# Kernel optimization log

Measured on AMD Instinct MI355X. Metric: run time of the kernel, lower is better.

Reference implementation:

```python
import jax, jax.numpy as jnp
import numpy as np

B, T = 256, 64
STOCH, DETER, HIDDEN = 32, 1024, 1024
EMBED, ACT, ENS = 1536, 6, 5
MIN_STD = 0.1
UPDATE_BIAS = -1.0
LN_EPS = 1e-5


def _layernorm(x, g, b):
    m = jnp.mean(x, -1, keepdims=True)
    v = jnp.var(x, -1, keepdims=True)
    return (x - m) * jax.lax.rsqrt(v + LN_EPS) * g + b


def setup_inputs() -> dict:
    key = jax.random.key(0)
    ks = jax.random.split(key, 24)
    s = 0.02
    return {
        "embed": jax.random.normal(ks[0], (B, T, EMBED), jnp.float32),
        "action": jax.random.normal(ks[1], (B, T, ACT), jnp.float32),
        "eps_post": jax.random.normal(ks[2], (B, T, STOCH), jnp.float32),
        "eps_prior": jax.random.normal(ks[3], (B, T, STOCH), jnp.float32),
        "is_first": jnp.zeros((B, T), bool),
        "ens_idx": jax.random.randint(ks[4], (T,), 0, ENS, jnp.int32),
        # GRU cell: Linear(hidden+deter -> 3*deter) + LayerNorm(3*deter)
        "W_gru": s * jax.random.normal(ks[5], (HIDDEN + DETER, 3 * DETER), jnp.float32),
        "b_gru": jnp.zeros((3 * DETER,), jnp.float32),
        "ln_g": jnp.ones((3 * DETER,), jnp.float32),
        "ln_b": jnp.zeros((3 * DETER,), jnp.float32),
        # img_inp: Linear(stoch+act -> hidden)
        "W_inp": s * jax.random.normal(ks[6], (STOCH + ACT, HIDDEN), jnp.float32),
        "b_inp": jnp.zeros((HIDDEN,), jnp.float32),
        # obs_out: Linear(deter+embed -> hidden)
        "W_obs": s * jax.random.normal(ks[7], (DETER + EMBED, HIDDEN), jnp.float32),
        "b_obs": jnp.zeros((HIDDEN,), jnp.float32),
        # ensemble img_out heads: Linear(deter -> hidden) x ENS
        "W_ens": s * jax.random.normal(ks[8], (ENS, DETER, HIDDEN), jnp.float32),
        "b_ens": jnp.zeros((ENS, HIDDEN), jnp.float32),
        # dist layers: Linear(hidden -> 2*stoch)
        "W_obs_dist": s * jax.random.normal(ks[9], (HIDDEN, 2 * STOCH), jnp.float32),
        "b_obs_dist": jnp.zeros((2 * STOCH,), jnp.float32),
        "W_ens_dist": s * jax.random.normal(ks[10], (ENS, HIDDEN, 2 * STOCH), jnp.float32),
        "b_ens_dist": jnp.zeros((ENS, 2 * STOCH), jnp.float32),
    }


def _observe(embed, action, eps_post, eps_prior, is_first, ens_idx,
             W_gru, b_gru, ln_g, ln_b, W_inp, b_inp, W_obs, b_obs,
             W_ens, b_ens, W_obs_dist, b_obs_dist, W_ens_dist, b_ens_dist):
    def step(carry, xs):
        stoch, deter = carry
        a_t, e_t, ep_t, eq_t, first_t, idx_t = xs
        m = (~first_t).astype(stoch.dtype)[:, None]  # mask previous state on episode start
        stoch, deter, a_t = stoch * m, deter * m, a_t * m
        # img_step: input MLP + GRU cell
        x = jax.nn.elu(jnp.concatenate([stoch, a_t], -1) @ W_inp + b_inp)  # [B,H]
        parts = _layernorm(jnp.concatenate([x, deter], -1) @ W_gru + b_gru, ln_g, ln_b)
        reset, cand, update = jnp.split(parts, 3, -1)
        reset = jax.nn.sigmoid(reset)
        cand = jnp.tanh(reset * cand)
        update = jax.nn.sigmoid(update + UPDATE_BIAS)
        deter_new = update * cand + (1.0 - update) * deter  # [B,DETER]
        # prior stats from randomly selected ensemble head (index chosen per step)
        h = jax.nn.elu(deter_new @ W_ens[idx_t] + b_ens[idx_t])
        pm, ps = jnp.split(h @ W_ens_dist[idx_t] + b_ens_dist[idx_t], 2, -1)
        ps = jax.nn.softplus(ps) + MIN_STD
        prior_stoch = pm + ps * ep_t
        # posterior from deter + embed
        xo = jax.nn.elu(jnp.concatenate([deter_new, e_t], -1) @ W_obs + b_obs)
        om, os = jnp.split(xo @ W_obs_dist + b_obs_dist, 2, -1)
        os = jax.nn.softplus(os) + MIN_STD
        post_stoch = om + os * eq_t
        out = jnp.concatenate([om, os, post_stoch, pm, ps, prior_stoch, deter_new], -1)
        return (post_stoch, deter_new), out

    tm = lambda x: jnp.swapaxes(x, 0, 1)  # batch-major -> time-major
    carry0 = (jnp.zeros((B, STOCH), embed.dtype), jnp.zeros((B, DETER), embed.dtype))
    xs = (tm(action), tm(embed), tm(eps_prior), tm(eps_post), is_first.T, ens_idx)
    _, out = jax.lax.scan(step, carry0, xs)
    return jnp.swapaxes(out, 0, 1)  # [B, T, 6*STOCH + DETER]


def reference(embed, action, eps_post, eps_prior, is_first, ens_idx,
              W_gru, b_gru, ln_g, ln_b, W_inp, b_inp, W_obs, b_obs,
              W_ens, b_ens, W_obs_dist, b_obs_dist, W_ens_dist, b_ens_dist):
    return _observe(embed, action, eps_post, eps_prior, is_first, ens_idx,
                    W_gru, b_gru, ln_g, ln_b, W_inp, b_inp, W_obs, b_obs,
                    W_ens, b_ens, W_obs_dist, b_obs_dist, W_ens_dist, b_ens_dist)
```

## Files before the change

kernel.cpp:

```cpp
#include <hip/hip_runtime.h>
#include <hip/hip_bf16.h>


#define B_ 256
#define T_ 64
#define STOCH_ 32
#define DETER_ 1024
#define HIDDEN_ 1024
#define EMBED_ 1536
#define ACT_ 6
#define OUTW_ 1216

typedef __attribute__((ext_vector_type(8))) short bf16x8;
typedef __attribute__((ext_vector_type(4))) float f32x4;

__device__ inline unsigned short f2bf(float x) {
    union { float f; unsigned int u; } v; v.f = x;
    unsigned int r = v.u + 0x7fffu + ((v.u >> 16) & 1u);
    return (unsigned short)(r >> 16);
}
__device__ inline float bf2f(unsigned short h) {
    union { unsigned int u; float f; } v; v.u = ((unsigned int)h) << 16;
    return v.f;
}
__device__ inline float softplus_f(float x) { return x > 20.f ? x : log1pf(expf(x)); }
__device__ inline float sigmoid_f(float x) { return 1.f / (1.f + expf(-x)); }
__device__ inline float elu_f(float x) { return x > 0.f ? x : expm1f(x); }

__global__ __launch_bounds__(256)
void k_transpose_cvt(const float* __restrict__ src, unsigned short* __restrict__ dst,
                     int K, int N) {
    __shared__ float tile[32][33];
    size_t off = (size_t)blockIdx.z * K * N;
    src += off; dst += off;
    int n0 = blockIdx.x * 32, k0 = blockIdx.y * 32;
    int tx = threadIdx.x, ty = threadIdx.y;
    for (int i = ty; i < 32; i += 8) tile[i][tx] = src[(size_t)(k0 + i) * N + n0 + tx];
    __syncthreads();
    for (int i = ty; i < 32; i += 8) dst[(size_t)(n0 + i) * K + k0 + tx] = f2bf(tile[tx][i]);
}

template<int MF, int NF, int KI>
__device__ inline void mfma_tile_db(const unsigned short* __restrict__ A, int lda,
                                    const unsigned short* __restrict__ Bt, int ldb,
                                    int row0, int col0, f32x4 acc[MF][NF]) {
    int lane = threadIdx.x & 63;
    int lr = lane & 15, q = lane >> 4;
    const unsigned short* ap = A + (size_t)(row0 + lr) * lda + q * 8;
    const unsigned short* bp = Bt + (size_t)(col0 + lr) * ldb + q * 8;
    bf16x8 a0[MF], b0[NF], a1[MF], b1[NF], a2[MF], b2[NF];
    auto ld = [&](bf16x8 (&av)[MF], bf16x8 (&bv)[NF], int kk) {
#pragma unroll
        for (int i = 0; i < MF; i++) av[i] = *(const bf16x8*)(ap + (size_t)i * 16 * lda + kk);
#pragma unroll
        for (int j = 0; j < NF; j++) bv[j] = *(const bf16x8*)(bp + (size_t)j * 16 * ldb + kk);
    };
    auto mm = [&](bf16x8 (&av)[MF], bf16x8 (&bv)[NF]) {
#pragma unroll
        for (int i = 0; i < MF; i++)
#pragma unroll
            for (int j = 0; j < NF; j++)
                acc[i][j] = __builtin_amdgcn_mfma_f32_16x16x32_bf16(av[i], bv[j], acc[i][j], 0, 0, 0);
    };
    ld(a0, b0, 0);
    if (KI > 1) ld(a1, b1, 32);
#pragma unroll
    for (int s = 0; s < KI; s++) {
        if (s + 2 < KI) {
            const int ml = (s + 2) % 3;
            if (ml == 0) ld(a0, b0, (s + 2) * 32);
            else if (ml == 1) ld(a1, b1, (s + 2) * 32);
            else ld(a2, b2, (s + 2) * 32);
        }
        const int mc = s % 3;
        if (mc == 0) mm(a0, b0);
        else if (mc == 1) mm(a1, b1);
        else mm(a2, b2);
    }
}

__global__ __launch_bounds__(256)
void k_gru(const unsigned short* __restrict__ xcat, const unsigned short* __restrict__ Wt,
           float* __restrict__ Gp) {
    int wave = threadIdx.x >> 6, lane = threadIdx.x & 63;
    int row0 = blockIdx.y * 128 + wave * 32, col0 = blockIdx.x * 32;
    int ks = blockIdx.z;
    f32x4 acc[2][2];
#pragma unroll
    for (int i = 0; i < 2; i++)
#pragma unroll
        for (int j = 0; j < 2; j++) { f32x4 z = {0.f, 0.f, 0.f, 0.f}; acc[i][j] = z; }
    mfma_tile_db<2, 2, 16>(xcat + ks * 512, 2048, Wt + ks * 512, 2048, row0, col0, acc);
    float* dst = Gp + (size_t)ks * (256 * 3072);
    int lr = lane & 15, q = lane >> 4;
#pragma unroll
    for (int i = 0; i < 2; i++)
#pragma unroll
        for (int j = 0; j < 2; j++)
#pragma unroll
            for (int r = 0; r < 4; r++) {
                int row = row0 + i * 16 + q * 4 + r;
                int col = col0 + j * 16 + lr;
                dst[(size_t)row * 3072 + col] = acc[i][j][r];
            }
}

__global__ __launch_bounds__(1024)
void k_gates(int t, const float* __restrict__ Gp, const float* __restrict__ b_gru,
             const float* __restrict__ ln_g, const float* __restrict__ ln_b,
             const float* __restrict__ deter_m, float* __restrict__ deter,
             unsigned short* __restrict__ dnew_bf, unsigned short* __restrict__ dcat,
             float* __restrict__ out) {
    int b = blockIdx.x, j = threadIdx.x;
    size_t base = (size_t)b * 3072 + j;
    float g0 = b_gru[j], g1 = b_gru[j + 1024], g2 = b_gru[j + 2048];
#pragma unroll
    for (int s = 0; s < 4; s++) {
        const float* p = Gp + (size_t)s * (256 * 3072) + base;
        g0 += p[0]; g1 += p[1024]; g2 += p[2048];
    }
    float s1 = g0 + g1 + g2;
    float s2 = g0 * g0 + g1 * g1 + g2 * g2;
#pragma unroll
    for (int o = 32; o > 0; o >>= 1) { s1 += __shfl_down(s1, o, 64); s2 += __shfl_down(s2, o, 64); }
    __shared__ float r1[16], r2[16];
    __shared__ float mean_s, rstd_s;
    int w = j >> 6;
    if ((j & 63) == 0) { r1[w] = s1; r2[w] = s2; }
    __syncthreads();
    if (j == 0) {
        float a = 0.f, c = 0.f;
        for (int i = 0; i < 16; i++) { a += r1[i]; c += r2[i]; }
        float mean = a / 3072.f;
        float var = c / 3072.f - mean * mean;
        mean_s = mean; rstd_s = rsqrtf(var + 1e-5f);
    }
    __syncthreads();
    float mean = mean_s, rstd = rstd_s;
    float n0 = (g0 - mean) * rstd * ln_g[j] + ln_b[j];
    float n1 = (g1 - mean) * rstd * ln_g[j + 1024] + ln_b[j + 1024];
    float n2 = (g2 - mean) * rstd * ln_g[j + 2048] + ln_b[j + 2048];
    float reset = sigmoid_f(n0);
    float cand = tanhf(reset * n1);
    float upd = sigmoid_f(n2 - 1.f);
    float dn = upd * cand + (1.f - upd) * deter_m[(size_t)b * 1024 + j];
    deter[(size_t)b * 1024 + j] = dn;
    dnew_bf[(size_t)b * 1024 + j] = f2bf(dn);
    dcat[(size_t)b * 2560 + j] = f2bf(dn);
    out[((size_t)b * T_ + t) * OUTW_ + 192 + j] = dn;
}

__global__ __launch_bounds__(256)
void k_heads(int t, const int* __restrict__ ens_idx,
             const unsigned short* __restrict__ dnew_bf, const unsigned short* __restrict__ dcat,
             const unsigned short* __restrict__ Wt_ens, const unsigned short* __restrict__ Wt_obs,
             float* __restrict__ h_part, float* __restrict__ xo_part) {
    int wave = threadIdx.x >> 6, lane = threadIdx.x & 63;
    int row0 = blockIdx.y * 128 + wave * 32, col0 = blockIdx.x * 32;
    int z = blockIdx.z;
    f32x4 acc[2][2];
#pragma unroll
    for (int i = 0; i < 2; i++)
#pragma unroll
        for (int j = 0; j < 2; j++) { f32x4 zz = {0.f, 0.f, 0.f, 0.f}; acc[i][j] = zz; }
    float* dst;
    if (z < 4) {
        int e = ens_idx[t];
        mfma_tile_db<2, 2, 8>(dnew_bf + z * 256, 1024,
                              Wt_ens + (size_t)e * 1024 * 1024 + z * 256, 1024, row0, col0, acc);
        dst = h_part + (size_t)z * (256 * 1024);
    } else {
        int zz = z - 4;
        mfma_tile_db<2, 2, 20>(dcat + zz * 640, 2560, Wt_obs + zz * 640, 2560, row0, col0, acc);
        dst = xo_part + (size_t)zz * (256 * 1024);
    }
    int lr = lane & 15, q = lane >> 4;
#pragma unroll
    for (int i = 0; i < 2; i++)
#pragma unroll
        for (int j = 0; j < 2; j++)
#pragma unroll
            for (int r = 0; r < 4; r++) {
                int row = row0 + i * 16 + q * 4 + r;
                int col = col0 + j * 16 + lr;
                dst[(size_t)row * 1024 + col] = acc[i][j][r];
            }
}

__global__ __launch_bounds__(256)
void k_dist_prep(int t,
                 const float* __restrict__ eps_post, const float* __restrict__ eps_prior,
                 const int* __restrict__ ens_idx,
                 const float* __restrict__ Wed, const float* __restrict__ bed,
                 const float* __restrict__ Wod, const float* __restrict__ bod,
                 const float* __restrict__ h_part, const float* __restrict__ xo_part,
                 const float* __restrict__ b_ens, const float* __restrict__ b_obs,
                 const float* __restrict__ action, const float* __restrict__ embed,
                 const unsigned char* __restrict__ is_first,
                 const float* __restrict__ W_inp, const float* __restrict__ b_inp,
                 float* __restrict__ stoch, const float* __restrict__ deter,
                 float* __restrict__ deter_m, unsigned short* __restrict__ xcat,
                 unsigned short* __restrict__ dcat, float* __restrict__ out) {
    __shared__ float s_h[1024], s_xo[1024], s_par[256], s_acc[128], s_stoch[32], s_am[8];
    int b = blockIdx.x, tid = threadIdx.x;
    if (t >= 0) {
        int e = ens_idx[t];
        {
            int i = tid * 4;
            const float* hb = h_part + (size_t)b * 1024 + i;
            f32x4 hv = *(const f32x4*)(hb);
            hv += *(const f32x4*)(hb + 1 * 256 * 1024);
            hv += *(const f32x4*)(hb + 2 * 256 * 1024);
            hv += *(const f32x4*)(hb + 3 * 256 * 1024);
            f32x4 hbia = *(const f32x4*)(b_ens + (size_t)e * 1024 + i);
            const float* xb = xo_part + (size_t)b * 1024 + i;
            f32x4 xv = *(const f32x4*)(xb);
            xv += *(const f32x4*)(xb + 1 * 256 * 1024);
            xv += *(const f32x4*)(xb + 2 * 256 * 1024);
            xv += *(const f32x4*)(xb + 3 * 256 * 1024);
            f32x4 xbia = *(const f32x4*)(b_obs + i);
#pragma unroll
            for (int r = 0; r < 4; r++) {
                s_h[i + r] = elu_f(hv[r] + hbia[r]);
                s_xo[i + r] = elu_f(xv[r] + xbia[r]);
            }
        }
        __syncthreads();
        {
            int kh = tid >> 7, c = tid & 127;
            int k0 = kh * 512;
            float acc = 0.f;
            if (c < 64) {
                const float* W = Wed + (size_t)e * 65536 + c;
                for (int k = 0; k < 512; k++) acc += s_h[k0 + k] * W[(size_t)(k0 + k) * 64];
            } else {
                const float* W = Wod + (c - 64);
                for (int k = 0; k < 512; k++) acc += s_xo[k0 + k] * W[(size_t)(k0 + k) * 64];
            }
            s_par[tid] = acc;
        }
        __syncthreads();
        if (tid < 128) {
            int c = tid & 63;
            float acc = s_par[tid] + s_par[tid + 128];
            acc += (tid < 64) ? bed[e * 64 + c] : bod[c];
            s_acc[tid] = acc;
        }
        __syncthreads();
        if (tid < 32) {
            float pm = s_acc[tid];
            float ps = softplus_f(s_acc[32 + tid]) + 0.1f;
            float om = s_acc[64 + tid];
            float os = softplus_f(s_acc[96 + tid]) + 0.1f;
            size_t bt = (size_t)b * T_ + t;
            float prior = pm + ps * eps_prior[bt * 32 + tid];
            float post = om + os * eps_post[bt * 32 + tid];
            float* o = out + bt * OUTW_;
            o[tid] = om; o[32 + tid] = os; o[64 + tid] = post;
            o[96 + tid] = pm; o[128 + tid] = ps; o[160 + tid] = prior;
            stoch[b * 32 + tid] = post;
            s_stoch[tid] = post;
        }
    } else {
        if (tid < 32) s_stoch[tid] = stoch[b * 32 + tid];
    }
    int tn = t + 1;
    if (tn < T_) {
        __syncthreads();
        float m = is_first[b * T_ + tn] ? 0.f : 1.f;
        if (tid < ACT_) s_am[tid] = action[((size_t)b * T_ + tn) * ACT_ + tid] * m;
        __syncthreads();
        for (int n = tid; n < 1024; n += 256) {
            float sacc = 0.f;
#pragma unroll
            for (int k = 0; k < 32; k++) sacc += s_stoch[k] * W_inp[k * 1024 + n];
            float a = b_inp[n] + m * sacc;
#pragma unroll
            for (int k = 0; k < ACT_; k++) a += s_am[k] * W_inp[(32 + k) * 1024 + n];
            xcat[(size_t)b * 2048 + n] = f2bf(elu_f(a));
            float dm = deter[(size_t)b * 1024 + n] * m;
            deter_m[(size_t)b * 1024 + n] = dm;
            xcat[(size_t)b * 2048 + 1024 + n] = f2bf(dm);
        }
        for (int j = tid; j < EMBED_; j += 256)
            dcat[(size_t)b * 2560 + 1024 + j] = f2bf(embed[((size_t)b * T_ + tn) * EMBED_ + j]);
    }
}

extern "C" void kernel_launch(void* const* d_in, const int* in_sizes, int n_in,
                              void* d_out, int out_size, void* d_ws, size_t ws_size,
                              hipStream_t stream) {
    const float* embed      = (const float*)d_in[0];
    const float* action     = (const float*)d_in[1];
    const float* eps_post   = (const float*)d_in[2];
    const float* eps_prior  = (const float*)d_in[3];
    const unsigned char* is_first = (const unsigned char*)d_in[4];
    const int* ens_idx      = (const int*)d_in[5];
    const float* W_gru      = (const float*)d_in[6];
    const float* b_gru      = (const float*)d_in[7];
    const float* ln_g       = (const float*)d_in[8];
    const float* ln_b       = (const float*)d_in[9];
    const float* W_inp      = (const float*)d_in[10];
    const float* b_inp      = (const float*)d_in[11];
    const float* W_obs      = (const float*)d_in[12];
    const float* b_obs      = (const float*)d_in[13];
    const float* W_ens      = (const float*)d_in[14];
    const float* b_ens      = (const float*)d_in[15];
    const float* W_obs_dist = (const float*)d_in[16];
    const float* b_obs_dist = (const float*)d_in[17];
    const float* W_ens_dist = (const float*)d_in[18];
    const float* b_ens_dist = (const float*)d_in[19];
    float* out = (float*)d_out;

    char* p = (char*)d_ws;
    auto take = [&](size_t bytes) -> char* {
        char* r = p;
        p += (bytes + 255) & ~(size_t)255;
        return r;
    };
    unsigned short* Wt_gru = (unsigned short*)take((size_t)3072 * 2048 * 2);
    unsigned short* Wt_obs = (unsigned short*)take((size_t)1024 * 2560 * 2);
    unsigned short* Wt_ens = (unsigned short*)take((size_t)5 * 1024 * 1024 * 2);
    float* deter   = (float*)take((size_t)B_ * 1024 * 4);
    float* stoch   = (float*)take((size_t)B_ * 32 * 4);
    float* deter_m = (float*)take((size_t)B_ * 1024 * 4);
    unsigned short* xcat    = (unsigned short*)take((size_t)B_ * 2048 * 2);
    unsigned short* dcat    = (unsigned short*)take((size_t)B_ * 2560 * 2);
    float* Gp = (float*)take((size_t)4 * B_ * 3072 * 4);
    unsigned short* dnew_bf = (unsigned short*)take((size_t)B_ * 1024 * 2);
    if ((size_t)(p - (char*)d_ws) > ws_size) return;
    float* h_part  = Gp;
    float* xo_part = Gp + (size_t)4 * B_ * 1024;

    hipMemsetAsync(deter, 0, (size_t)B_ * 1024 * 4 + (size_t)B_ * 32 * 4, stream);

    k_transpose_cvt<<<dim3(96, 64, 1), dim3(32, 8), 0, stream>>>(W_gru, Wt_gru, 2048, 3072);
    k_transpose_cvt<<<dim3(32, 80, 1), dim3(32, 8), 0, stream>>>(W_obs, Wt_obs, 2560, 1024);
    k_transpose_cvt<<<dim3(32, 32, 5), dim3(32, 8), 0, stream>>>(W_ens, Wt_ens, 1024, 1024);

    k_dist_prep<<<dim3(B_), dim3(256), 0, stream>>>(-1, eps_post, eps_prior, ens_idx,
        W_ens_dist, b_ens_dist, W_obs_dist, b_obs_dist, h_part, xo_part, b_ens, b_obs,
        action, embed, is_first, W_inp, b_inp, stoch, deter, deter_m, xcat, dcat, out);

    for (int t = 0; t < T_; ++t) {
        k_gru<<<dim3(96, 2, 4), dim3(256), 0, stream>>>(xcat, Wt_gru, Gp);
        k_gates<<<dim3(B_), dim3(1024), 0, stream>>>(t, Gp, b_gru, ln_g, ln_b, deter_m, deter,
                                                     dnew_bf, dcat, out);
        k_heads<<<dim3(32, 2, 8), dim3(256), 0, stream>>>(t, ens_idx, dnew_bf, dcat,
                                                          Wt_ens, Wt_obs, h_part, xo_part);
        k_dist_prep<<<dim3(B_), dim3(256), 0, stream>>>(t, eps_post, eps_prior, ens_idx,
            W_ens_dist, b_ens_dist, W_obs_dist, b_obs_dist, h_part, xo_part, b_ens, b_obs,
            action, embed, is_first, W_inp, b_inp, stoch, deter, deter_m, xcat, dcat, out);
    }
}
```

Measured before the change: 4.846 ms.

## Precompute embed projection of obs_out for all timesteps outside the recurrence

Splits the obs_out matmul into a deter part and an embed part. The embed part (embed @ W_obs[1024:]) does not depend on the recurrent state, so one large batched GEMM computes it for all timesteps before the loop, and the result is stored as bf16. The per-step obs head now contracts only over the 1024 deter dimensions, and the per-step copy of embed into dcat is removed. k_dist_prep also moves to 512 threads, and the stoch buffer and initial memset are replaced by zero-initialisation when t<0. This costs an extra workspace of about B*T*(1536+1024) bf16 and rounds the embed projection to bf16.

```diff
diff --git a/kernel.cpp b/kernel.cpp
--- a/kernel.cpp
+++ b/kernel.cpp
@@ -4,11 +4,8 @@
 
 #define B_ 256
 #define T_ 64
-#define STOCH_ 32
-#define DETER_ 1024
-#define HIDDEN_ 1024
+#define ACT_ 6
 #define EMBED_ 1536
-#define ACT_ 6
 #define OUTW_ 1216
 
 typedef __attribute__((ext_vector_type(8))) short bf16x8;
@@ -26,6 +23,15 @@
 __device__ inline float softplus_f(float x) { return x > 20.f ? x : log1pf(expf(x)); }
 __device__ inline float sigmoid_f(float x) { return 1.f / (1.f + expf(-x)); }
 __device__ inline float elu_f(float x) { return x > 0.f ? x : expm1f(x); }
+
+__global__ __launch_bounds__(256)
+void k_convert(const float* __restrict__ src, unsigned short* __restrict__ dst, long n4) {
+    for (long i = blockIdx.x * 256 + threadIdx.x; i < n4; i += (long)gridDim.x * 256) {
+        f32x4 v = *(const f32x4*)(src + i * 4);
+        unsigned short* d = dst + i * 4;
+        d[0] = f2bf(v[0]); d[1] = f2bf(v[1]); d[2] = f2bf(v[2]); d[3] = f2bf(v[3]);
+    }
+}
 
 __global__ __launch_bounds__(256)
 void k_transpose_cvt(const float* __restrict__ src, unsigned short* __restrict__ dst,
@@ -80,6 +86,30 @@
 }
 
 __global__ __launch_bounds__(256)
+void k_eobs(const unsigned short* __restrict__ ebf, const unsigned short* __restrict__ Wt_obs,
+            unsigned short* __restrict__ Eobs) {
+    int wave = threadIdx.x >> 6, lane = threadIdx.x & 63;
+    int row0 = blockIdx.y * 128 + wave * 32, col0 = blockIdx.x * 32;
+    f32x4 acc[2][2];
+#pragma unroll
+    for (int i = 0; i < 2; i++)
+#pragma unroll
+        for (int j = 0; j < 2; j++) { f32x4 z = {0.f, 0.f, 0.f, 0.f}; acc[i][j] = z; }
+    mfma_tile_db<2, 2, 48>(ebf, 1536, Wt_obs + 1024, 2560, row0, col0, acc);
+    int lr = lane & 15, q = lane >> 4;
+#pragma unroll
+    for (int i = 0; i < 2; i++)
+#pragma unroll
+        for (int j = 0; j < 2; j++)
+#pragma unroll
+            for (int r = 0; r < 4; r++) {
+                int row = row0 + i * 16 + q * 4 + r;
+                int col = col0 + j * 16 + lr;
+                Eobs[(size_t)row * 1024 + col] = f2bf(acc[i][j][r]);
+            }
+}
+
+__global__ __launch_bounds__(256)
 void k_gru(const unsigned short* __restrict__ xcat, const unsigned short* __restrict__ Wt,
            float* __restrict__ Gp) {
     int wave = threadIdx.x >> 6, lane = threadIdx.x & 63;
@@ -109,8 +139,7 @@
 void k_gates(int t, const float* __restrict__ Gp, const float* __restrict__ b_gru,
              const float* __restrict__ ln_g, const float* __restrict__ ln_b,
              const float* __restrict__ deter_m, float* __restrict__ deter,
-             unsigned short* __restrict__ dnew_bf, unsigned short* __restrict__ dcat,
-             float* __restrict__ out) {
+             unsigned short* __restrict__ dnew_bf, float* __restrict__ out) {
     int b = blockIdx.x, j = threadIdx.x;
     size_t base = (size_t)b * 3072 + j;
     float g0 = b_gru[j], g1 = b_gru[j + 1024], g2 = b_gru[j + 2048];
@@ -146,13 +175,12 @@
     float dn = upd * cand + (1.f - upd) * deter_m[(size_t)b * 1024 + j];
     deter[(size_t)b * 1024 + j] = dn;
     dnew_bf[(size_t)b * 1024 + j] = f2bf(dn);
-    dcat[(size_t)b * 2560 + j] = f2bf(dn);
     out[((size_t)b * T_ + t) * OUTW_ + 192 + j] = dn;
 }
 
 __global__ __launch_bounds__(256)
 void k_heads(int t, const int* __restrict__ ens_idx,
-             const unsigned short* __restrict__ dnew_bf, const unsigned short* __restrict__ dcat,
+             const unsigned short* __restrict__ dnew_bf,
              const unsigned short* __restrict__ Wt_ens, const unsigned short* __restrict__ Wt_obs,
              float* __restrict__ h_part, float* __restrict__ xo_part) {
     int wave = threadIdx.x >> 6, lane = threadIdx.x & 63;
@@ -171,7 +199,8 @@
         dst = h_part + (size_t)z * (256 * 1024);
     } else {
         int zz = z - 4;
-        mfma_tile_db<2, 2, 20>(dcat + zz * 640, 2560, Wt_obs + zz * 640, 2560, row0, col0, acc);
+        mfma_tile_db<2, 2, 8>(dnew_bf + zz * 256, 1024,
+                              Wt_obs + zz * 256, 2560, row0, col0, acc);
         dst = xo_part + (size_t)zz * (256 * 1024);
     }
     int lr = lane & 15, q = lane >> 4;
@@ -187,62 +216,60 @@
             }
 }
 
-__global__ __launch_bounds__(256)
+__global__ __launch_bounds__(512)
 void k_dist_prep(int t,
                  const float* __restrict__ eps_post, const float* __restrict__ eps_prior,
                  const int* __restrict__ ens_idx,
                  const float* __restrict__ Wed, const float* __restrict__ bed,
                  const float* __restrict__ Wod, const float* __restrict__ bod,
                  const float* __restrict__ h_part, const float* __restrict__ xo_part,
+                 const unsigned short* __restrict__ Eobs,
                  const float* __restrict__ b_ens, const float* __restrict__ b_obs,
-                 const float* __restrict__ action, const float* __restrict__ embed,
+                 const float* __restrict__ action,
                  const unsigned char* __restrict__ is_first,
                  const float* __restrict__ W_inp, const float* __restrict__ b_inp,
-                 float* __restrict__ stoch, const float* __restrict__ deter,
+                 const float* __restrict__ deter,
                  float* __restrict__ deter_m, unsigned short* __restrict__ xcat,
-                 unsigned short* __restrict__ dcat, float* __restrict__ out) {
-    __shared__ float s_h[1024], s_xo[1024], s_par[256], s_acc[128], s_stoch[32], s_am[8];
+                 float* __restrict__ out) {
+    __shared__ float s_h[1024], s_xo[1024], s_par[512], s_acc[128], s_stoch[32], s_am[8];
     int b = blockIdx.x, tid = threadIdx.x;
     if (t >= 0) {
         int e = ens_idx[t];
         {
-            int i = tid * 4;
-            const float* hb = h_part + (size_t)b * 1024 + i;
-            f32x4 hv = *(const f32x4*)(hb);
-            hv += *(const f32x4*)(hb + 1 * 256 * 1024);
-            hv += *(const f32x4*)(hb + 2 * 256 * 1024);
-            hv += *(const f32x4*)(hb + 3 * 256 * 1024);
-            f32x4 hbia = *(const f32x4*)(b_ens + (size_t)e * 1024 + i);
-            const float* xb = xo_part + (size_t)b * 1024 + i;
-            f32x4 xv = *(const f32x4*)(xb);
-            xv += *(const f32x4*)(xb + 1 * 256 * 1024);
-            xv += *(const f32x4*)(xb + 2 * 256 * 1024);
-            xv += *(const f32x4*)(xb + 3 * 256 * 1024);
-            f32x4 xbia = *(const f32x4*)(b_obs + i);
-#pragma unroll
-            for (int r = 0; r < 4; r++) {
-                s_h[i + r] = elu_f(hv[r] + hbia[r]);
-                s_xo[i + r] = elu_f(xv[r] + xbia[r]);
-            }
+            int i = tid * 2;
+            float h0 = b_ens[(size_t)e * 1024 + i], h1 = b_ens[(size_t)e * 1024 + i + 1];
+            float x0 = b_obs[i], x1 = b_obs[i + 1];
+            size_t bt1024 = ((size_t)b * T_ + (t >= 0 ? t : 0)) * 1024;
+            x0 += bf2f(Eobs[bt1024 + i]);
+            x1 += bf2f(Eobs[bt1024 + i + 1]);
+#pragma unroll
+            for (int s = 0; s < 4; s++) {
+                const float* hb = h_part + (size_t)s * (256 * 1024) + (size_t)b * 1024 + i;
+                h0 += hb[0]; h1 += hb[1];
+                const float* xb = xo_part + (size_t)s * (256 * 1024) + (size_t)b * 1024 + i;
+                x0 += xb[0]; x1 += xb[1];
+            }
+            s_h[i] = elu_f(h0); s_h[i + 1] = elu_f(h1);
+            s_xo[i] = elu_f(x0); s_xo[i + 1] = elu_f(x1);
         }
         __syncthreads();
         {
-            int kh = tid >> 7, c = tid & 127;
-            int k0 = kh * 512;
+            int kq = tid >> 7, c = tid & 127;
+            int k0 = kq * 256;
             float acc = 0.f;
             if (c < 64) {
                 const float* W = Wed + (size_t)e * 65536 + c;
-                for (int k = 0; k < 512; k++) acc += s_h[k0 + k] * W[(size_t)(k0 + k) * 64];
+                for (int k = 0; k < 256; k++) acc += s_h[k0 + k] * W[(size_t)(k0 + k) * 64];
             } else {
                 const float* W = Wod + (c - 64);
-                for (int k = 0; k < 512; k++) acc += s_xo[k0 + k] * W[(size_t)(k0 + k) * 64];
+                for (int k = 0; k < 256; k++) acc += s_xo[k0 + k] * W[(size_t)(k0 + k) * 64];
             }
             s_par[tid] = acc;
         }
         __syncthreads();
         if (tid < 128) {
             int c = tid & 63;
-            float acc = s_par[tid] + s_par[tid + 128];
+            float acc = s_par[tid] + s_par[tid + 128] + s_par[tid + 256] + s_par[tid + 384];
             acc += (tid < 64) ? bed[e * 64 + c] : bod[c];
             s_acc[tid] = acc;
         }
@@ -258,11 +285,10 @@
             float* o = out + bt * OUTW_;
             o[tid] = om; o[32 + tid] = os; o[64 + tid] = post;
             o[96 + tid] = pm; o[128 + tid] = ps; o[160 + tid] = prior;
-            stoch[b * 32 + tid] = post;
             s_stoch[tid] = post;
         }
     } else {
-        if (tid < 32) s_stoch[tid] = stoch[b * 32 + tid];
+        if (tid < 32) s_stoch[tid] = 0.f;
     }
     int tn = t + 1;
     if (tn < T_) {
@@ -270,7 +296,7 @@
         float m = is_first[b * T_ + tn] ? 0.f : 1.f;
         if (tid < ACT_) s_am[tid] = action[((size_t)b * T_ + tn) * ACT_ + tid] * m;
         __syncthreads();
-        for (int n = tid; n < 1024; n += 256) {
+        for (int n = tid; n < 1024; n += 512) {
             float sacc = 0.f;
 #pragma unroll
             for (int k = 0; k < 32; k++) sacc += s_stoch[k] * W_inp[k * 1024 + n];
@@ -278,12 +304,11 @@
 #pragma unroll
             for (int k = 0; k < ACT_; k++) a += s_am[k] * W_inp[(32 + k) * 1024 + n];
             xcat[(size_t)b * 2048 + n] = f2bf(elu_f(a));
-            float dm = deter[(size_t)b * 1024 + n] * m;
+            float dv = (t >= 0) ? deter[(size_t)b * 1024 + n] : 0.f;
+            float dm = dv * m;
             deter_m[(size_t)b * 1024 + n] = dm;
             xcat[(size_t)b * 2048 + 1024 + n] = f2bf(dm);
         }
-        for (int j = tid; j < EMBED_; j += 256)
-            dcat[(size_t)b * 2560 + 1024 + j] = f2bf(embed[((size_t)b * T_ + tn) * EMBED_ + j]);
     }
 }
 
@@ -322,34 +347,34 @@
     unsigned short* Wt_obs = (unsigned short*)take((size_t)1024 * 2560 * 2);
     unsigned short* Wt_ens = (unsigned short*)take((size_t)5 * 1024 * 1024 * 2);
     float* deter   = (float*)take((size_t)B_ * 1024 * 4);
-    float* stoch   = (float*)take((size_t)B_ * 32 * 4);
     float* deter_m = (float*)take((size_t)B_ * 1024 * 4);
     unsigned short* xcat    = (unsigned short*)take((size_t)B_ * 2048 * 2);
-    unsigned short* dcat    = (unsigned short*)take((size_t)B_ * 2560 * 2);
     float* Gp = (float*)take((size_t)4 * B_ * 3072 * 4);
     unsigned short* dnew_bf = (unsigned short*)take((size_t)B_ * 1024 * 2);
+    unsigned short* ebf  = (unsigned short*)take((size_t)B_ * T_ * EMBED_ * 2);
+    unsigned short* Eobs = (unsigned short*)take((size_t)B_ * T_ * 1024 * 2);
     if ((size_t)(p - (char*)d_ws) > ws_size) return;
     float* h_part  = Gp;
     float* xo_part = Gp + (size_t)4 * B_ * 1024;
 
-    hipMemsetAsync(deter, 0, (size_t)B_ * 1024 * 4 + (size_t)B_ * 32 * 4, stream);
-
     k_transpose_cvt<<<dim3(96, 64, 1), dim3(32, 8), 0, stream>>>(W_gru, Wt_gru, 2048, 3072);
     k_transpose_cvt<<<dim3(32, 80, 1), dim3(32, 8), 0, stream>>>(W_obs, Wt_obs, 2560, 1024);
     k_transpose_cvt<<<dim3(32, 32, 5), dim3(32, 8), 0, stream>>>(W_ens, Wt_ens, 1024, 1024);
-
-    k_dist_prep<<<dim3(B_), dim3(256), 0, stream>>>(-1, eps_post, eps_prior, ens_idx,
-        W_ens_dist, b_ens_dist, W_obs_dist, b_obs_dist, h_part, xo_part, b_ens, b_obs,
-        action, embed, is_first, W_inp, b_inp, stoch, deter, deter_m, xcat, dcat, out);
+    k_convert<<<dim3(2048), dim3(256), 0, stream>>>(embed, ebf, (long)B_ * T_ * EMBED_ / 4);
+    k_eobs<<<dim3(32, 128), dim3(256), 0, stream>>>(ebf, Wt_obs, Eobs);
+
+    k_dist_prep<<<dim3(B_), dim3(512), 0, stream>>>(-1, eps_post, eps_prior, ens_idx,
+        W_ens_dist, b_ens_dist, W_obs_dist, b_obs_dist, h_part, xo_part, Eobs, b_ens, b_obs,
+        action, is_first, W_inp, b_inp, deter, deter_m, xcat, out);
 
     for (int t = 0; t < T_; ++t) {
         k_gru<<<dim3(96, 2, 4), dim3(256), 0, stream>>>(xcat, Wt_gru, Gp);
         k_gates<<<dim3(B_), dim3(1024), 0, stream>>>(t, Gp, b_gru, ln_g, ln_b, deter_m, deter,
-                                                     dnew_bf, dcat, out);
-        k_heads<<<dim3(32, 2, 8), dim3(256), 0, stream>>>(t, ens_idx, dnew_bf, dcat,
+                                                     dnew_bf, out);
+        k_heads<<<dim3(32, 2, 8), dim3(256), 0, stream>>>(t, ens_idx, dnew_bf,
                                                           Wt_ens, Wt_obs, h_part, xo_part);
-        k_dist_prep<<<dim3(B_), dim3(256), 0, stream>>>(t, eps_post, eps_prior, ens_idx,
-            W_ens_dist, b_ens_dist, W_obs_dist, b_obs_dist, h_part, xo_part, b_ens, b_obs,
-            action, embed, is_first, W_inp, b_inp, stoch, deter, deter_m, xcat, dcat, out);
-    }
-}
+        k_dist_prep<<<dim3(B_), dim3(512), 0, stream>>>(t, eps_post, eps_prior, ens_idx,
+            W_ens_dist, b_ens_dist, W_obs_dist, b_obs_dist, h_part, xo_part, Eobs, b_ens, b_obs,
+            action, is_first, W_inp, b_inp, deter, deter_m, xcat, out);
+    }
+}
```

Result: faster. 4.316 ms (-10.9%).
